# Performance work log

Hardware: AMD Instinct MI355X
Metric: run time of the kernel (lower is better)

## Reference

```python
import jax, jax.numpy as jnp
import numpy as np

NUM_HEADS = 32
NUM_KV_HEADS = 8
HEAD_DIM = 64
ROPE_THETA = 10000.0


def setup_inputs() -> dict:
    key = jax.random.key(0)
    ks = jax.random.split(key, 5)
    B, N, D = 2, 2048, 2048
    kv_out = NUM_KV_HEADS * HEAD_DIM
    s = 0.02
    return {
        "x": jax.random.normal(ks[0], (B, N, D), dtype=jnp.float32),
        "Wq": jax.random.normal(ks[1], (D, D), dtype=jnp.float32) * s,
        "Wk": jax.random.normal(ks[2], (kv_out, D), dtype=jnp.float32) * s,
        "Wv": jax.random.normal(ks[3], (kv_out, D), dtype=jnp.float32) * s,
        "Wo": jax.random.normal(ks[4], (D, D), dtype=jnp.float32) * s,
    }


def _rotate_half(t):
    d = t.shape[-1] // 2
    return jnp.concatenate([-t[..., d:], t[..., :d]], axis=-1)


def _rope_cos_sin(N, dtype):
    # Llama rotary embedding: inv_freq over even dims, duplicated along last axis
    inv_freq = 1.0 / (ROPE_THETA ** (jnp.arange(0, HEAD_DIM, 2, dtype=jnp.float32) / HEAD_DIM))
    freqs = jnp.arange(N, dtype=jnp.float32)[:, None] * inv_freq[None, :]  # [N, hd/2]
    emb = jnp.concatenate([freqs, freqs], axis=-1)  # [N, hd]
    return jnp.cos(emb).astype(dtype), jnp.sin(emb).astype(dtype)


def reference(x, Wq, Wk, Wv, Wo):
    B, N, D = x.shape
    groups = NUM_HEADS // NUM_KV_HEADS
    scale = HEAD_DIM ** -0.5

    q = (x @ Wq.T).reshape(B, N, NUM_HEADS, HEAD_DIM).transpose(0, 2, 1, 3)      # [B,H,N,hd]
    k = (x @ Wk.T).reshape(B, N, NUM_KV_HEADS, HEAD_DIM).transpose(0, 2, 1, 3)   # [B,KVH,N,hd]
    v = (x @ Wv.T).reshape(B, N, NUM_KV_HEADS, HEAD_DIM).transpose(0, 2, 1, 3)

    cos, sin = _rope_cos_sin(N, x.dtype)  # [N,hd]
    cos = cos[None, None]  # [1,1,N,hd]
    sin = sin[None, None]
    q = q * cos + _rotate_half(q) * sin
    k = k * cos + _rotate_half(k) * sin

    # repeat_kv: [B,KVH,N,hd] -> [B,H,N,hd]
    k = jnp.repeat(k, groups, axis=1)
    v = jnp.repeat(v, groups, axis=1)

    attn = jnp.einsum('bhqd,bhkd->bhqk', q, k) * scale  # [B,H,N,N]
    attn = jax.nn.softmax(attn, axis=-1)
    out = jnp.einsum('bhqk,bhkd->bhqd', attn, v)        # [B,H,N,hd]
    out = out.transpose(0, 2, 1, 3).reshape(B, N, D)
    return out @ Wo.T
```

## Files before the change

kernel.cpp:

```cpp
#include <hip/hip_runtime.h>
#include <hip/hip_bf16.h>

#define Bc 2
#define Nc 2048
#define Dc 2048
#define Hc 32
#define KVHc 8

typedef __attribute__((ext_vector_type(4))) float f32x4;
typedef __attribute__((ext_vector_type(8))) short short8;

__device__ __forceinline__ ushort f2b(float f) {
  union { float f; unsigned u; } v; v.f = f;
  unsigned u = v.u;
  unsigned r = (u + 0x7FFFu + ((u >> 16) & 1u)) >> 16;
  return (ushort)r;
}
__device__ __forceinline__ float b2f(ushort h) {
  union { unsigned u; float f; } v; v.u = ((unsigned)h) << 16; return v.f;
}

__device__ __forceinline__ float fexp2(float x) {
  float r;
  asm("v_exp_f32 %0, %1" : "=v"(r) : "v"(x));
  return r;
}

__device__ __forceinline__ unsigned cvt_pk_bf16(float lo, float hi) {
  unsigned r;
  asm("v_cvt_pk_bf16_f32 %0, %1, %2" : "=v"(r) : "v"(lo), "v"(hi));
  return r;
}

__device__ __forceinline__ void gload_lds16(const ushort* g, ushort* l) {
  __builtin_amdgcn_global_load_lds(
      (const __attribute__((address_space(1))) void*)g,
      (__attribute__((address_space(3))) void*)l, 16, 0, 0);
}

template<int ITERS>
__device__ __forceinline__ void stage_tile(const ushort* gbase, int gstride,
                                           ushort* lds, int tid) {
  #pragma unroll
  for (int i = 0; i < ITERS; ++i) {
    int s = i * 256 + tid;
    int row = s >> 3;
    int sch = (s & 7) ^ (row & 7);
    gload_lds16(gbase + (size_t)row * gstride + sch * 8, lds + s * 8);
  }
}
__device__ __forceinline__ short8 read_frag(const ushort* lds, int row, int kbyte) {
  int off = kbyte ^ ((row & 7) << 4);
  return *(const short8*)((const char*)lds + row * 128 + off);
}

__device__ __forceinline__ int f_attn(int row) {
  return ((row >> 1) & 1) | (((row >> 3) & 1) << 1) |
         ((((row >> 2) ^ (row >> 4)) & 1) << 2);
}

__global__ void k_convert_all(
    const float* __restrict__ x,  const float* __restrict__ wq,
    const float* __restrict__ wk, const float* __restrict__ wv,
    const float* __restrict__ wo, ushort* __restrict__ xb,
    ushort* __restrict__ wqkv, ushort* __restrict__ wob) {
  int i = blockIdx.x * 256 + threadIdx.x;
  const float* src; ushort* dst; int off;
  if (i < 2097152)      { src = x;  dst = xb;             off = i; }
  else if (i < 3145728) { src = wq; dst = wqkv;           off = i - 2097152; }
  else if (i < 3407872) { src = wk; dst = wqkv + 4194304; off = i - 3145728; }
  else if (i < 3670016) { src = wv; dst = wqkv + 5242880; off = i - 3407872; }
  else                  { src = wo; dst = wob;            off = i - 3670016; }
  float4 v = ((const float4*)src)[off];
  ushort4 o;
  o.x = f2b(v.x); o.y = f2b(v.y); o.z = f2b(v.z); o.w = f2b(v.w);
  *(ushort4*)&dst[(size_t)off * 4] = o;
}

__global__ void k_rope_table(float* __restrict__ cosT, float* __restrict__ sinT) {
  int i = blockIdx.x * 256 + threadIdx.x;
  int n = i >> 5, f = i & 31;
  float inv = powf(10000.0f, -(float)f * (1.0f / 32.0f));
  float ang = (float)n * inv;
  cosT[i] = cosf(ang);
  sinT[i] = sinf(ang);
}

__global__ __launch_bounds__(512, 2) void k_gemm8(
    const ushort* __restrict__ A, const ushort* __restrict__ Bm,
    ushort* __restrict__ C, int M, int Nn, int K) {
  __shared__ ushort lds[2][2][2][128 * 64];
  int nt = Nn >> 8;
  int bid = blockIdx.x;
  int m0 = (bid / nt) << 8, n0 = (bid % nt) << 8;
  int tid = threadIdx.x;
  int lane = tid & 63, w = tid >> 6;
  int wr = w >> 2, wc = w & 3;
  int lc = lane & 15, lq = lane >> 4;
  int nkt = K >> 6, nit = nkt >> 1;

  const ushort* Ag = A + (size_t)m0 * K;
  const ushort* Bg = Bm + (size_t)n0 * K;

  int r0s = tid >> 3;
  int sch = (tid & 7) ^ (r0s & 7);
  size_t g0 = (size_t)r0s * K + sch * 8;
  size_t g1 = (size_t)(64 + r0s) * K + sch * 8;
  int l0 = tid * 8, l1 = 4096 + tid * 8;

  int sw = (lc & 7) << 4;
  int koff0 = (lq * 16) ^ sw;
  int koff1 = (64 + lq * 16) ^ sw;
  int abase = lc * 128;
  int bbase = ((wc & 1) * 64 + lc) * 128;

  f32x4 acc[8][4];
  #pragma unroll
  for (int r = 0; r < 8; ++r)
    #pragma unroll
    for (int c = 0; c < 4; ++c) acc[r][c] = (f32x4){0.f, 0.f, 0.f, 0.f};
  short8 afr[4][2], bfr[4][2];

  auto STAGE = [&](int op, int h, int t) {
    if (t >= nkt) t -= nkt;
    const ushort* gb = (op ? Bg : Ag) + (size_t)(h * 128) * K + t * 64;
    ushort* lb = &lds[t & 1][op][h][0];
    gload_lds16(gb + g0, lb + l0);
    gload_lds16(gb + g1, lb + l1);
  };
  auto LDA = [&](int b, int mh) {
    const char* p = (const char*)&lds[b][0][wr][0];
    #pragma unroll
    for (int mi = 0; mi < 4; ++mi) {
      int rb = abase + (mh * 4 + mi) * 2048;
      afr[mi][0] = *(const short8*)(p + rb + koff0);
      afr[mi][1] = *(const short8*)(p + rb + koff1);
    }
  };
  auto LDB = [&](int b, int nh) {
    const char* p = (const char*)&lds[b][1][wc >> 1][0];
    #pragma unroll
    for (int ni = 0; ni < 2; ++ni) {
      int rb = bbase + (nh * 2 + ni) * 2048;
      bfr[nh * 2 + ni][0] = *(const short8*)(p + rb + koff0);
      bfr[nh * 2 + ni][1] = *(const short8*)(p + rb + koff1);
    }
  };
  auto MFMA16 = [&](int mh, int nh) {
    __builtin_amdgcn_s_setprio(1);
    #pragma unroll
    for (int mi = 0; mi < 4; ++mi)
      #pragma unroll
      for (int ni = 0; ni < 2; ++ni) {
        f32x4 a = acc[mh * 4 + mi][nh * 2 + ni];
        a = __builtin_amdgcn_mfma_f32_16x16x32_bf16(afr[mi][0], bfr[nh * 2 + ni][0], a, 0, 0, 0);
        a = __builtin_amdgcn_mfma_f32_16x16x32_bf16(afr[mi][1], bfr[nh * 2 + ni][1], a, 0, 0, 0);
        acc[mh * 4 + mi][nh * 2 + ni] = a;
      }
    __builtin_amdgcn_s_setprio(0);
  };

  #define BAR __builtin_amdgcn_s_barrier()
  #define LGK do { asm volatile("s_waitcnt lgkmcnt(0)" ::: "memory"); \
                   __builtin_amdgcn_sched_barrier(0); } while (0)
  #define VM4 asm volatile("s_waitcnt vmcnt(4)" ::: "memory")

  STAGE(1, 0, 0); STAGE(0, 0, 0); STAGE(0, 1, 0); STAGE(1, 1, 0);
  STAGE(1, 0, 1); STAGE(1, 1, 1);
  VM4; BAR;

  for (int i = 0; i < nit; ++i) {
    int t1 = 2 * i + 1;
    LDA(0, 0); LDB(0, 0); STAGE(0, 0, t1);
    BAR; LGK; MFMA16(0, 0); BAR;
    LDB(0, 1); STAGE(0, 1, t1);
    BAR; LGK; MFMA16(0, 1); BAR;
    LDA(0, 1); STAGE(1, 0, t1 + 1);
    BAR; LGK; MFMA16(1, 1); BAR;
    STAGE(0, 0, t1 + 1);
    BAR; MFMA16(1, 0); VM4; BAR;
    LDA(1, 0); LDB(1, 0); STAGE(0, 1, t1 + 1);
    BAR; LGK; MFMA16(0, 0); BAR;
    LDB(1, 1); STAGE(1, 1, t1 + 1);
    BAR; LGK; MFMA16(0, 1); BAR;
    LDA(1, 1); STAGE(1, 0, t1 + 2);
    BAR; LGK; MFMA16(1, 1); BAR;
    STAGE(1, 1, t1 + 2);
    BAR; MFMA16(1, 0); VM4; BAR;
  }
  #undef BAR
  #undef LGK
  #undef VM4

  #pragma unroll
  for (int mf = 0; mf < 8; ++mf)
    #pragma unroll
    for (int nf = 0; nf < 4; ++nf) {
      int gr = m0 + wr * 128 + mf * 16 + lq * 4;
      int gc = n0 + wc * 64 + nf * 16 + lc;
      #pragma unroll
      for (int e = 0; e < 4; ++e)
        C[(size_t)(gr + e) * Nn + gc] = f2b(acc[mf][nf][e]);
    }
}

template<typename TOUT>
__global__ __launch_bounds__(256) void k_gemm_bt(
    const ushort* __restrict__ A, const ushort* __restrict__ Bm,
    TOUT* __restrict__ C, int M, int Nn, int K) {
  __shared__ ushort ldsA[128 * 64];
  __shared__ ushort ldsB[128 * 64];
  int nt = Nn >> 7;
  int m0 = (int)(blockIdx.x / nt) << 7;
  int n0 = (int)(blockIdx.x % nt) << 7;
  int tid = threadIdx.x;
  int lane = tid & 63, w = tid >> 6;
  int wr = w >> 1, wc = w & 1;
  int lc = lane & 15, lq = lane >> 4;
  f32x4 acc[4][4];
  #pragma unroll
  for (int r = 0; r < 4; ++r)
    #pragma unroll
    for (int c = 0; c < 4; ++c) acc[r][c] = (f32x4){0.f, 0.f, 0.f, 0.f};
  int nkt = K >> 6;
  for (int kt = 0; kt < nkt; ++kt) {
    stage_tile<4>(A + (size_t)m0 * K + kt * 64, K, ldsA, tid);
    stage_tile<4>(Bm + (size_t)n0 * K + kt * 64, K, ldsB, tid);
    __syncthreads();
    #pragma unroll
    for (int kk = 0; kk < 2; ++kk) {
      int kbyte = kk * 64 + lq * 16;
      short8 af[4], bfr[4];
      #pragma unroll
      for (int r = 0; r < 4; ++r) af[r] = read_frag(ldsA, wr * 64 + r * 16 + lc, kbyte);
      #pragma unroll
      for (int c = 0; c < 4; ++c) bfr[c] = read_frag(ldsB, wc * 64 + c * 16 + lc, kbyte);
      #pragma unroll
      for (int r = 0; r < 4; ++r)
        #pragma unroll
        for (int c = 0; c < 4; ++c)
          acc[r][c] = __builtin_amdgcn_mfma_f32_16x16x32_bf16(af[r], bfr[c], acc[r][c], 0, 0, 0);
    }
    __syncthreads();
  }
  #pragma unroll
  for (int r = 0; r < 4; ++r)
    #pragma unroll
    for (int c = 0; c < 4; ++c) {
      int gr = m0 + wr * 64 + r * 16 + lq * 4;
      int gc = n0 + wc * 64 + c * 16 + lc;
      #pragma unroll
      for (int e = 0; e < 4; ++e) {
        float val = acc[r][c][e];
        if constexpr (sizeof(TOUT) == 2)
          C[(size_t)(gr + e) * Nn + gc] = f2b(val);
        else
          C[(size_t)(gr + e) * Nn + gc] = val;
      }
    }
}

__global__ void k_rope_qk(const ushort* __restrict__ qkv,
                          const float* __restrict__ cosT, const float* __restrict__ sinT,
                          ushort* __restrict__ qr, ushort* __restrict__ kr) {
  const float QS = 0.125f * 1.44269504089f;
  int bn = blockIdx.x;
  int b = bn >> 11, n = bn & (Nc - 1);
  int t = threadIdx.x;
  const ushort* row = qkv + (size_t)bn * 3072;
  #pragma unroll
  for (int i = 0; i < 4; ++i) {
    int p = i * 256 + t;
    int h = p >> 5, dp = p & 31;
    float c = cosT[n * 32 + dp], s = sinT[n * 32 + dp];
    float q0 = b2f(row[h * 64 + dp]);
    float q1 = b2f(row[h * 64 + dp + 32]);
    size_t ob = ((size_t)(b * Hc + h) * Nc + n) * 64 + dp;
    qr[ob]      = f2b((q0 * c - q1 * s) * QS);
    qr[ob + 32] = f2b((q1 * c + q0 * s) * QS);
  }
  {
    int kvh = t >> 5, dp = t & 31;
    float c = cosT[n * 32 + dp], s = sinT[n * 32 + dp];
    float k0 = b2f(row[2048 + kvh * 64 + dp]);
    float k1 = b2f(row[2048 + kvh * 64 + dp + 32]);
    size_t ob = ((size_t)(b * KVHc + kvh) * Nc + n) * 64 + dp;
    kr[ob]      = f2b(k0 * c - k1 * s);
    kr[ob + 32] = f2b(k1 * c + k0 * s);
  }
}

__global__ void k_transpose_v(const ushort* __restrict__ qkv, ushort* __restrict__ vt) {
  __shared__ ushort tile[64][72];
  int bid = blockIdx.x;
  int ntile = bid & 31, kvh = (bid >> 5) & 7, b = bid >> 8;
  int t = threadIdx.x;
  int n0 = ntile * 64;
  #pragma unroll
  for (int i = 0; i < 4; ++i) {
    int s = i * 256 + t;
    int r = s >> 4, c4 = s & 15;
    ushort4 v = *(const ushort4*)&qkv[(size_t)(b * Nc + n0 + r) * 3072 + 2560 + kvh * 64 + c4 * 4];
    tile[r][c4 * 4 + 0] = v.x; tile[r][c4 * 4 + 1] = v.y;
    tile[r][c4 * 4 + 2] = v.z; tile[r][c4 * 4 + 3] = v.w;
  }
  __syncthreads();
  #pragma unroll
  for (int i = 0; i < 4; ++i) {
    int s = i * 256 + t;
    int d = s >> 4, c4 = s & 15;
    ushort4 v;
    v.x = tile[c4 * 4 + 0][d]; v.y = tile[c4 * 4 + 1][d];
    v.z = tile[c4 * 4 + 2][d]; v.w = tile[c4 * 4 + 3][d];
    *(ushort4*)&vt[(size_t)((b * KVHc + kvh) * 64 + d) * Nc + n0 + c4 * 4] = v;
  }
}

__global__ __launch_bounds__(512) void k_attn(
    const ushort* __restrict__ qr, const ushort* __restrict__ kr,
    const ushort* __restrict__ vt, ushort* __restrict__ ctx) {
  __shared__ ushort ldsK[2][64 * 64];
  __shared__ ushort ldsV[2][64 * 64];
  int bid = blockIdx.x;
  int qt = bid & 31, p = (bid >> 5) & 1, kvh = (bid >> 6) & 7, b = bid >> 9;
  int tid = threadIdx.x;
  int w = tid >> 6, lane = tid & 63;
  int lc = lane & 15, lq = lane >> 4;
  int h = kvh * 4 + p * 2 + (w >> 2);
  int q0 = qt * 64 + (w & 3) * 16;
  const ushort* Qb = qr + (size_t)(b * Hc + h) * Nc * 64;
  const ushort* Kb = kr + (size_t)(b * KVHc + kvh) * Nc * 64;
  const ushort* Vb = vt + (size_t)(b * KVHc + kvh) * 64 * Nc;
  short8 aq[2];
  #pragma unroll
  for (int kk = 0; kk < 2; ++kk)
    aq[kk] = *(const short8*)&Qb[(size_t)(q0 + lc) * 64 + kk * 32 + lq * 8];

  int offK[2][4], offV[2][4];
  #pragma unroll
  for (int c = 0; c < 4; ++c) {
    int rowK = ((c >> 1) << 5) + ((lc >> 2) << 3) + ((c & 1) << 2) + (lc & 3);
    int fs = f_attn(rowK) << 4;
    #pragma unroll
    for (int kk = 0; kk < 2; ++kk)
      offK[kk][c] = rowK * 128 + ((kk * 64 + lq * 16) ^ fs);
  }
  #pragma unroll
  for (int dd = 0; dd < 4; ++dd) {
    int rowV = dd * 16 + lc;
    int fs = f_attn(rowV) << 4;
    #pragma unroll
    for (int kk = 0; kk < 2; ++kk)
      offV[kk][dd] = rowV * 128 + ((kk * 64 + lq * 16) ^ fs);
  }

  int r0 = tid >> 3;
  int c0 = (tid & 7) ^ f_attn(r0);
  int oK0 = r0 * 64 + c0 * 8;
  int oV0 = r0 * Nc + c0 * 8;
  int d0 = tid * 8;

  f32x4 oacc[4];
  #pragma unroll
  for (int d = 0; d < 4; ++d) oacc[d] = (f32x4){0.f, 0.f, 0.f, 0.f};
  float lpart = 0.f;

  auto compute = [&](const ushort* lK, const ushort* lV) {
    f32x4 sc[4];
    __builtin_amdgcn_s_setprio(1);
    #pragma unroll
    for (int c = 0; c < 4; ++c) {
      f32x4 a = (f32x4){0.f, 0.f, 0.f, 0.f};
      #pragma unroll
      for (int kk = 0; kk < 2; ++kk)
        a = __builtin_amdgcn_mfma_f32_16x16x32_bf16(
            *(const short8*)((const char*)lK + offK[kk][c]), aq[kk], a, 0, 0, 0);
      sc[c] = a;
    }
    __builtin_amdgcn_s_setprio(0);
    float ps[4];
    #pragma unroll
    for (int c = 0; c < 4; ++c) {
      #pragma unroll
      for (int e = 0; e < 4; ++e)
        sc[c][e] = fexp2(sc[c][e]);
      ps[c] = (sc[c][0] + sc[c][1]) + (sc[c][2] + sc[c][3]);
    }
    lpart += (ps[0] + ps[1]) + (ps[2] + ps[3]);
    unsigned pk[4][2];
    #pragma unroll
    for (int c = 0; c < 4; ++c) {
      pk[c][0] = cvt_pk_bf16(sc[c][0], sc[c][1]);
      pk[c][1] = cvt_pk_bf16(sc[c][2], sc[c][3]);
    }
    __builtin_amdgcn_s_setprio(1);
    #pragma unroll
    for (int kk = 0; kk < 2; ++kk) {
      union { short8 s; unsigned u[4]; } pa;
      pa.u[0] = pk[2 * kk][0];
      pa.u[1] = pk[2 * kk][1];
      pa.u[2] = pk[2 * kk + 1][0];
      pa.u[3] = pk[2 * kk + 1][1];
      #pragma unroll
      for (int dd = 0; dd < 4; ++dd)
        oacc[dd] = __builtin_amdgcn_mfma_f32_16x16x32_bf16(
            *(const short8*)((const char*)lV + offV[kk][dd]), pa.s, oacc[dd], 0, 0, 0);
    }
    __builtin_amdgcn_s_setprio(0);
  };

  gload_lds16(Kb + oK0, &ldsK[0][d0]);
  gload_lds16(Vb + oV0, &ldsV[0][d0]);
  oK0 += 4096; oV0 += 64;
  __syncthreads();

  constexpr int NT = Nc / 64;
  for (int t2 = 0; t2 < NT; t2 += 2) {
    gload_lds16(Kb + oK0, &ldsK[1][d0]);
    gload_lds16(Vb + oV0, &ldsV[1][d0]);
    oK0 += 4096; oV0 += 64;
    compute(ldsK[0], ldsV[0]);
    __syncthreads();
    if (t2 + 2 < NT) {
      gload_lds16(Kb + oK0, &ldsK[0][d0]);
      gload_lds16(Vb + oV0, &ldsV[0][d0]);
    }
    oK0 += 4096; oV0 += 64;
    compute(ldsK[1], ldsV[1]);
    __syncthreads();
  }
  float lrun = lpart;
  lrun += __shfl_xor(lrun, 16, 64);
  lrun += __shfl_xor(lrun, 32, 64);
  float rinv = 1.f / lrun;
  #pragma unroll
  for (int dd = 0; dd < 4; ++dd) {
    ushort4 o;
    o.x = f2b(oacc[dd][0] * rinv);
    o.y = f2b(oacc[dd][1] * rinv);
    o.z = f2b(oacc[dd][2] * rinv);
    o.w = f2b(oacc[dd][3] * rinv);
    *(ushort4*)&ctx[(size_t)(b * Nc + q0 + lc) * Dc + h * 64 + dd * 16 + lq * 4] = o;
  }
}

extern "C" void kernel_launch(void* const* d_in, const int* in_sizes, int n_in,
                              void* d_out, int out_size, void* d_ws, size_t ws_size,
                              hipStream_t stream) {
  const float* x  = (const float*)d_in[0];
  const float* Wq = (const float*)d_in[1];
  const float* Wk = (const float*)d_in[2];
  const float* Wv = (const float*)d_in[3];
  const float* Wo = (const float*)d_in[4];

  ushort* ws   = (ushort*)d_ws;
  ushort* xb   = ws;
  ushort* wqkv = xb + 8388608;
  ushort* wob  = wqkv + 6291456;
  float*  cosT = (float*)(wob + 4194304);
  float*  sinT = cosT + 65536;
  ushort* qkv  = (ushort*)(sinT + 65536);
  ushort* qr   = qkv + 12582912;
  ushort* kr   = qr + 8388608;
  ushort* vt   = kr + 2097152;
  ushort* ctx  = vt + 2097152;

  k_convert_all<<<18432, 256, 0, stream>>>(x, Wq, Wk, Wv, Wo, xb, wqkv, wob);
  k_rope_table<<<256, 256, 0, stream>>>(cosT, sinT);

  k_gemm8<<<192, 512, 0, stream>>>(xb, wqkv, qkv, 4096, 3072, 2048);
  k_rope_qk<<<4096, 256, 0, stream>>>(qkv, cosT, sinT, qr, kr);
  k_transpose_v<<<512, 256, 0, stream>>>(qkv, vt);
  k_attn<<<1024, 512, 0, stream>>>(qr, kr, vt, ctx);
  k_gemm_bt<float><<<512, 256, 0, stream>>>(ctx, wob, (float*)d_out, 4096, 2048, 2048);
}
```

Measured before the change: 208.8 us.

## Software-pipeline attention loop so PV of previous tile overlaps current exp

Restructures the attention main loop into a one-stage software pipeline. Each iteration issues the QK^T MFMAs for tile t, then runs the PV MFMAs for tile t-1 while the exp2 and bf16 packing for tile t follow. The aim is to overlap transcendental/VALU work with matrix-core work. The V buffer grows to a triple buffer because V for tile t-1 must stay resident, which adds LDS use and index rotation plus a drain step after the loop.

After: 222.9 us. 6.8% more time.

```diff
diff --git a/kernel.cpp b/kernel.cpp
--- a/kernel.cpp
+++ b/kernel.cpp
@@ -320,7 +320,7 @@
     const ushort* __restrict__ qr, const ushort* __restrict__ kr,
     const ushort* __restrict__ vt, ushort* __restrict__ ctx) {
   __shared__ ushort ldsK[2][64 * 64];
-  __shared__ ushort ldsV[2][64 * 64];
+  __shared__ ushort ldsV[3][64 * 64];
   int bid = blockIdx.x;
   int qt = bid & 31, p = (bid >> 5) & 1, kvh = (bid >> 6) & 7, b = bid >> 9;
   int tid = threadIdx.x;
@@ -364,47 +364,21 @@
   #pragma unroll
   for (int d = 0; d < 4; ++d) oacc[d] = (f32x4){0.f, 0.f, 0.f, 0.f};
   float lpart = 0.f;
-
-  auto compute = [&](const ushort* lK, const ushort* lV) {
-    f32x4 sc[4];
-    __builtin_amdgcn_s_setprio(1);
-    #pragma unroll
-    for (int c = 0; c < 4; ++c) {
-      f32x4 a = (f32x4){0.f, 0.f, 0.f, 0.f};
-      #pragma unroll
-      for (int kk = 0; kk < 2; ++kk)
-        a = __builtin_amdgcn_mfma_f32_16x16x32_bf16(
-            *(const short8*)((const char*)lK + offK[kk][c]), aq[kk], a, 0, 0, 0);
-      sc[c] = a;
-    }
-    __builtin_amdgcn_s_setprio(0);
-    float ps[4];
-    #pragma unroll
-    for (int c = 0; c < 4; ++c) {
-      #pragma unroll
-      for (int e = 0; e < 4; ++e)
-        sc[c][e] = fexp2(sc[c][e]);
-      ps[c] = (sc[c][0] + sc[c][1]) + (sc[c][2] + sc[c][3]);
-    }
-    lpart += (ps[0] + ps[1]) + (ps[2] + ps[3]);
-    unsigned pk[4][2];
-    #pragma unroll
-    for (int c = 0; c < 4; ++c) {
-      pk[c][0] = cvt_pk_bf16(sc[c][0], sc[c][1]);
-      pk[c][1] = cvt_pk_bf16(sc[c][2], sc[c][3]);
-    }
+  unsigned pkp[4][2];
+
+  auto PV = [&](const char* lV) {
     __builtin_amdgcn_s_setprio(1);
     #pragma unroll
     for (int kk = 0; kk < 2; ++kk) {
       union { short8 s; unsigned u[4]; } pa;
-      pa.u[0] = pk[2 * kk][0];
-      pa.u[1] = pk[2 * kk][1];
-      pa.u[2] = pk[2 * kk + 1][0];
-      pa.u[3] = pk[2 * kk + 1][1];
+      pa.u[0] = pkp[2 * kk][0];
+      pa.u[1] = pkp[2 * kk][1];
+      pa.u[2] = pkp[2 * kk + 1][0];
+      pa.u[3] = pkp[2 * kk + 1][1];
       #pragma unroll
       for (int dd = 0; dd < 4; ++dd)
         oacc[dd] = __builtin_amdgcn_mfma_f32_16x16x32_bf16(
-            *(const short8*)((const char*)lV + offV[kk][dd]), pa.s, oacc[dd], 0, 0, 0);
+            *(const short8*)(lV + offV[kk][dd]), pa.s, oacc[dd], 0, 0, 0);
     }
     __builtin_amdgcn_s_setprio(0);
   };
@@ -415,20 +389,46 @@
   __syncthreads();
 
   constexpr int NT = Nc / 64;
-  for (int t2 = 0; t2 < NT; t2 += 2) {
-    gload_lds16(Kb + oK0, &ldsK[1][d0]);
-    gload_lds16(Vb + oV0, &ldsV[1][d0]);
+  int vm1 = 2, v0 = 0, vp1 = 1;
+  for (int t = 0; t < NT; ++t) {
+    if (t + 1 < NT) {
+      gload_lds16(Kb + oK0, &ldsK[(t + 1) & 1][d0]);
+      gload_lds16(Vb + oV0, &ldsV[vp1][d0]);
+    }
     oK0 += 4096; oV0 += 64;
-    compute(ldsK[0], ldsV[0]);
+    const char* lK = (const char*)&ldsK[t & 1][0];
+    f32x4 sc[4];
+    __builtin_amdgcn_s_setprio(1);
+    #pragma unroll
+    for (int c = 0; c < 4; ++c) {
+      f32x4 a = (f32x4){0.f, 0.f, 0.f, 0.f};
+      #pragma unroll
+      for (int kk = 0; kk < 2; ++kk)
+        a = __builtin_amdgcn_mfma_f32_16x16x32_bf16(
+            *(const short8*)(lK + offK[kk][c]), aq[kk], a, 0, 0, 0);
+      sc[c] = a;
+    }
+    __builtin_amdgcn_s_setprio(0);
+    if (t > 0) PV((const char*)&ldsV[vm1][0]);
+    float ps[4];
+    #pragma unroll
+    for (int c = 0; c < 4; ++c) {
+      #pragma unroll
+      for (int e = 0; e < 4; ++e)
+        sc[c][e] = fexp2(sc[c][e]);
+      ps[c] = (sc[c][0] + sc[c][1]) + (sc[c][2] + sc[c][3]);
+    }
+    lpart += (ps[0] + ps[1]) + (ps[2] + ps[3]);
+    #pragma unroll
+    for (int c = 0; c < 4; ++c) {
+      pkp[c][0] = cvt_pk_bf16(sc[c][0], sc[c][1]);
+      pkp[c][1] = cvt_pk_bf16(sc[c][2], sc[c][3]);
+    }
     __syncthreads();
-    if (t2 + 2 < NT) {
-      gload_lds16(Kb + oK0, &ldsK[0][d0]);
-      gload_lds16(Vb + oV0, &ldsV[0][d0]);
-    }
-    oK0 += 4096; oV0 += 64;
-    compute(ldsK[1], ldsV[1]);
-    __syncthreads();
-  }
+    int tmp = vm1; vm1 = v0; v0 = vp1; vp1 = tmp;
+  }
+  PV((const char*)&ldsV[vm1][0]);
+
   float lrun = lpart;
   lrun += __shfl_xor(lrun, 16, 64);
   lrun += __shfl_xor(lrun, 32, 64);
```
